# Optimization experiments

Measured on AMD Instinct MI355X. Metric: run time of the kernel, lower is better.

Reference implementation:

```python
import jax, jax.numpy as jnp
import numpy as np

N = 50000      # nodes
E = 800000     # edges
IN = 128       # in_channels
C = 32         # hidden_channels per head
H = 8          # heads
NC = 2         # num_classes
EPS = 1e-5     # batchnorm eps
SLOPE = 0.2    # leaky relu negative slope


def setup_inputs() -> dict:
    key = jax.random.key(0)
    ks = jax.random.split(key, 16)
    d = {}
    d["x"] = jax.random.normal(ks[0], (N, IN), dtype=jnp.float32)
    d["edge_index"] = jax.random.randint(ks[1], (2, E), 0, N, dtype=jnp.int64)
    # layer 0: IN -> H*C (concat)
    s0 = 1.0 / np.sqrt(IN)
    d["Wl0"] = jax.random.normal(ks[2], (IN, H * C), dtype=jnp.float32) * s0
    d["Wr0"] = jax.random.normal(ks[3], (IN, H * C), dtype=jnp.float32) * s0
    d["att0"] = jax.random.normal(ks[4], (H, C), dtype=jnp.float32) * (1.0 / np.sqrt(C))
    d["b0"] = jnp.zeros((H * C,), dtype=jnp.float32)
    d["g0"] = jnp.ones((H * C,), dtype=jnp.float32)
    d["be0"] = jnp.zeros((H * C,), dtype=jnp.float32)
    d["m0"] = jax.random.normal(ks[5], (H * C,), dtype=jnp.float32) * 0.1
    d["v0"] = jax.random.uniform(ks[6], (H * C,), dtype=jnp.float32, minval=0.5, maxval=1.5)
    # layer 1: H*C -> C (mean over heads, concat=False)
    s1 = 1.0 / np.sqrt(H * C)
    d["Wl1"] = jax.random.normal(ks[7], (H * C, H * C), dtype=jnp.float32) * s1
    d["Wr1"] = jax.random.normal(ks[8], (H * C, H * C), dtype=jnp.float32) * s1
    d["att1"] = jax.random.normal(ks[9], (H, C), dtype=jnp.float32) * (1.0 / np.sqrt(C))
    d["b1"] = jnp.zeros((C,), dtype=jnp.float32)
    d["g1"] = jnp.ones((C,), dtype=jnp.float32)
    d["be1"] = jnp.zeros((C,), dtype=jnp.float32)
    d["m1"] = jax.random.normal(ks[10], (C,), dtype=jnp.float32) * 0.1
    d["v1"] = jax.random.uniform(ks[11], (C,), dtype=jnp.float32, minval=0.5, maxval=1.5)
    # classifier C -> NC
    d["Wc"] = jax.random.normal(ks[12], (C, NC), dtype=jnp.float32) * (1.0 / np.sqrt(C))
    d["bc"] = jnp.zeros((NC,), dtype=jnp.float32)
    return d


def _gatv2_layer(x, src, dst, Wl, Wr, att, b, concat, num_nodes):
    # GATv2Conv (PyG semantics): x_l = source proj, x_r = target proj,
    # e_ij = att . LeakyReLU(x_l[j] + x_r[i]); softmax over incoming edges of i;
    # out_i = sum_j alpha_ij * x_l[j]. Self-loops are added (PyG default).
    nH, nC = att.shape
    xl = (x @ Wl).reshape(num_nodes, nH, nC)
    xr = (x @ Wr).reshape(num_nodes, nH, nC)
    e = xl[src] + xr[dst]                              # [E', H, C]
    e = jnp.where(e > 0, e, SLOPE * e)
    logits = jnp.einsum('ehc,hc->eh', e, att)          # [E', H]
    m = jax.ops.segment_max(logits, dst, num_segments=num_nodes)   # [N, H]
    ex = jnp.exp(logits - m[dst])
    denom = jax.ops.segment_sum(ex, dst, num_segments=num_nodes)   # [N, H]
    alpha = ex / denom[dst]                            # [E', H]
    msg = alpha[:, :, None] * xl[src]                  # [E', H, C]
    out = jax.ops.segment_sum(msg, dst, num_segments=num_nodes)    # [N, H, C]
    if concat:
        return out.reshape(num_nodes, nH * nC) + b
    return out.mean(axis=1) + b


def _bn(x, g, be, m, v):
    return (x - m) * jax.lax.rsqrt(v + EPS) * g + be


def reference(x, edge_index, Wl0, Wr0, att0, b0, g0, be0, m0, v0,
              Wl1, Wr1, att1, b1, g1, be1, m1, v1, Wc, bc):
    num_nodes = x.shape[0]
    loop = jnp.arange(num_nodes, dtype=edge_index.dtype)
    src = jnp.concatenate([edge_index[0], loop])
    dst = jnp.concatenate([edge_index[1], loop])
    h = _gatv2_layer(x, src, dst, Wl0, Wr0, att0, b0, True, num_nodes)
    h = _bn(h, g0, be0, m0, v0)
    h = jax.nn.elu(h)   # eval mode: dropout is identity
    h = _gatv2_layer(h, src, dst, Wl1, Wr1, att1, b1, False, num_nodes)
    h = _bn(h, g1, be1, m1, v1)
    return h @ Wc + bc
```

## Files before the change

kernel.cpp:

```cpp
#include <hip/hip_runtime.h>
#include <math.h>

#define N_NODES 50000
#define M_PAD   50048
#define E_EDGES 800000
#define IN_CH   128
#define C_CH    32
#define H_HEADS 8
#define HC      256
#define BN_EPS  1e-5f
#define SLOPE   0.2f

#define SCAN_CHUNK 512
#define SCAN_B     ((N_NODES + SCAN_CHUNK - 1) / SCAN_CHUNK)

typedef _Float16 f16x8 __attribute__((ext_vector_type(8)));
typedef _Float16 f16x4 __attribute__((ext_vector_type(4)));
typedef _Float16 f16x2 __attribute__((ext_vector_type(2)));
typedef float    f32x4 __attribute__((ext_vector_type(4)));


__global__ void k_init_deg(int* deg, int n) {
    int i = blockIdx.x * blockDim.x + threadIdx.x;
    if (i < n) deg[i] = 1;
}

__global__ void k_hist(const int* __restrict__ dst, int* deg, int e) {
    int i = blockIdx.x * blockDim.x + threadIdx.x;
    if (i < e) atomicAdd(&deg[dst[i]], 1);
}

__global__ __launch_bounds__(256) void k_scan_local(
        const int* __restrict__ deg, int* __restrict__ row_ptr,
        int* __restrict__ partials, int n) {
    __shared__ int sm[256];
    int t = threadIdx.x;
    int base = blockIdx.x * SCAN_CHUNK;
    int i0 = base + 2 * t, i1 = i0 + 1;
    int a = (i0 < n) ? deg[i0] : 0;
    int b = (i1 < n) ? deg[i1] : 0;
    int s = a + b;
    sm[t] = s;
    __syncthreads();
    #pragma unroll
    for (int off = 1; off < 256; off <<= 1) {
        int u = (t >= off) ? sm[t - off] : 0;
        __syncthreads();
        sm[t] += u;
        __syncthreads();
    }
    int excl = sm[t] - s;
    if (i0 < n) row_ptr[i0] = excl;
    if (i1 < n) row_ptr[i1] = excl + a;
    if (t == 255) partials[blockIdx.x] = sm[255];
}

__global__ __launch_bounds__(128) void k_scan_part(
        int* __restrict__ partials, int* __restrict__ row_ptr_n) {
    __shared__ int sm[128];
    int t = threadIdx.x;
    int v = (t < SCAN_B) ? partials[t] : 0;
    sm[t] = v;
    __syncthreads();
    #pragma unroll
    for (int off = 1; off < 128; off <<= 1) {
        int u = (t >= off) ? sm[t - off] : 0;
        __syncthreads();
        sm[t] += u;
        __syncthreads();
    }
    if (t < SCAN_B) partials[t] = sm[t] - v;
    if (t == 127) *row_ptr_n = sm[127];
}

__global__ void k_scan_add(int* __restrict__ row_ptr, int* __restrict__ cursor,
                           const int* __restrict__ partials, int n) {
    int i = blockIdx.x * blockDim.x + threadIdx.x;
    if (i < n) {
        int v = row_ptr[i] + partials[i / SCAN_CHUNK];
        row_ptr[i] = v;
        cursor[i] = v;
    }
}

__global__ void k_fill(const int* __restrict__ src, const int* __restrict__ dst,
                       int* cursor, int* csr_src, int e, int n) {
    int i = blockIdx.x * blockDim.x + threadIdx.x;
    if (i < e) {
        int d = dst[i];
        int p = atomicAdd(&cursor[d], 1);
        csr_src[p] = src[i];
    } else if (i < e + n) {
        int v = i - e;
        int p = atomicAdd(&cursor[v], 1);
        csr_src[p] = v;
    }
}


__global__ void k_split_x(const float* __restrict__ x, _Float16* __restrict__ xf) {
    int t = blockIdx.x * blockDim.x + threadIdx.x;
    if (t >= M_PAD * (IN_CH / 4)) return;
    int row = t / (IN_CH / 4);
    float4 v = {0.f, 0.f, 0.f, 0.f};
    if (row < N_NODES) v = ((const float4*)x)[t];
    f16x4 h = { (_Float16)v.x, (_Float16)v.y, (_Float16)v.z, (_Float16)v.w };
    ((f16x4*)xf)[t] = h;
}

__global__ void k_split_w(const float* __restrict__ W,
                          _Float16* __restrict__ wh, _Float16* __restrict__ wl,
                          int K, int N) {
    int t = blockIdx.x * blockDim.x + threadIdx.x;
    if (t >= K * N) return;
    int n = t / K, k = t - n * K;
    float v = W[(size_t)k * N + n];
    _Float16 h = (_Float16)v;
    wh[t] = h;
    wl[t] = (_Float16)(v - (float)h);
}


#define BK  32
#define LDA 40

__global__ __launch_bounds__(256) void k_gemm_mfma(
        const _Float16* __restrict__ A,
        const _Float16* __restrict__ W0h, const _Float16* __restrict__ W0l,
        const _Float16* __restrict__ W1h, const _Float16* __restrict__ W1l,
        _Float16* __restrict__ C0, _Float16* __restrict__ C1, int K) {
    const _Float16* Wh = blockIdx.z ? W1h : W0h;
    const _Float16* Wl = blockIdx.z ? W1l : W0l;
    _Float16* C = blockIdx.z ? C1 : C0;
    __shared__ _Float16 As[128 * LDA];
    __shared__ _Float16 Bh[128 * LDA], Bl[128 * LDA];
    int t = threadIdx.x;
    int lane = t & 63, wv = t >> 6;
    int quad = lane >> 4, r16 = lane & 15;
    size_t mBase = (size_t)blockIdx.x * 128;
    size_t nBase = (size_t)blockIdx.y * 128;
    int sr = t >> 2;
    int sc = (t & 3) * 8;
    f32x4 acc[2][8] = {};
    for (int k0 = 0; k0 < K; k0 += BK) {
        const _Float16* gA  = A + (mBase + sr) * K + k0 + sc;
        const _Float16* gBh = Wh + (nBase + sr) * K + k0 + sc;
        const _Float16* gBl = Wl + (nBase + sr) * K + k0 + sc;
        *(f16x8*)&As[sr * LDA + sc]        = *(const f16x8*)gA;
        *(f16x8*)&As[(sr + 64) * LDA + sc] = *(const f16x8*)(gA + (size_t)64 * K);
        *(f16x8*)&Bh[sr * LDA + sc]        = *(const f16x8*)gBh;
        *(f16x8*)&Bh[(sr + 64) * LDA + sc] = *(const f16x8*)(gBh + (size_t)64 * K);
        *(f16x8*)&Bl[sr * LDA + sc]        = *(const f16x8*)gBl;
        *(f16x8*)&Bl[(sr + 64) * LDA + sc] = *(const f16x8*)(gBl + (size_t)64 * K);
        __syncthreads();
        f16x8 av[2];
        #pragma unroll
        for (int mi = 0; mi < 2; ++mi) {
            int m = wv * 32 + mi * 16 + r16;
            av[mi] = *(f16x8*)&As[m * LDA + quad * 8];
        }
        #pragma unroll
        for (int ni = 0; ni < 8; ++ni) {
            int n = ni * 16 + r16;
            f16x8 bhv = *(f16x8*)&Bh[n * LDA + quad * 8];
            f16x8 blv = *(f16x8*)&Bl[n * LDA + quad * 8];
            #pragma unroll
            for (int mi = 0; mi < 2; ++mi) {
                acc[mi][ni] = __builtin_amdgcn_mfma_f32_16x16x32_f16(av[mi], bhv, acc[mi][ni], 0, 0, 0);
                acc[mi][ni] = __builtin_amdgcn_mfma_f32_16x16x32_f16(av[mi], blv, acc[mi][ni], 0, 0, 0);
            }
        }
        __syncthreads();
    }
    #pragma unroll
    for (int mi = 0; mi < 2; ++mi)
        #pragma unroll
        for (int r = 0; r < 4; ++r) {
            size_t row = mBase + wv * 32 + mi * 16 + quad * 4 + r;
            _Float16* cp = C + row * 256 + nBase + r16;
            #pragma unroll
            for (int ni = 0; ni < 8; ++ni)
                cp[ni * 16] = (_Float16)acc[mi][ni][r];
        }
}


__device__ __forceinline__ float edge_w16(f16x4 h, f16x4 xr, f16x4 att) {
    f16x4 e = h + xr;
    f16x4 es = e * (_Float16)SLOPE;
    f16x4 l = __builtin_elementwise_max(e, es);
#if __has_builtin(__builtin_amdgcn_fdot2)
    f16x2 l01 = __builtin_shufflevector(l, l, 0, 1);
    f16x2 l23 = __builtin_shufflevector(l, l, 2, 3);
    f16x2 a01 = __builtin_shufflevector(att, att, 0, 1);
    f16x2 a23 = __builtin_shufflevector(att, att, 2, 3);
    float p = __builtin_amdgcn_fdot2(l01, a01, 0.f, false);
    p = __builtin_amdgcn_fdot2(l23, a23, p, false);
#else
    float p = (float)l[0] * (float)att[0];
    p = fmaf((float)l[1], (float)att[1], p);
    p = fmaf((float)l[2], (float)att[2], p);
    p = fmaf((float)l[3], (float)att[3], p);
#endif
    p += __shfl_xor(p, 1);
    p += __shfl_xor(p, 2);
    p += __shfl_xor(p, 4);
    return __expf(p);
}

__device__ __forceinline__ float4 edge_accum(
        const f16x4* __restrict__ xl4, f16x4 xr_h, f16x4 att_h,
        const int* __restrict__ csr_src, int beg, int end, int lane) {
    const f16x4* xlp = xl4 + lane;
    float4 acc = {0.f, 0.f, 0.f, 0.f};
    float S = 0.f;
    int j = beg;
    for (; j + 4 <= end; j += 4) {
        int s0 = csr_src[j];
        int s1 = csr_src[j + 1];
        int s2 = csr_src[j + 2];
        int s3 = csr_src[j + 3];
        f16x4 h0 = xlp[(size_t)s0 * 64];
        f16x4 h1 = xlp[(size_t)s1 * 64];
        f16x4 h2 = xlp[(size_t)s2 * 64];
        f16x4 h3 = xlp[(size_t)s3 * 64];
        float w0 = edge_w16(h0, xr_h, att_h);
        float w1 = edge_w16(h1, xr_h, att_h);
        float w2 = edge_w16(h2, xr_h, att_h);
        float w3 = edge_w16(h3, xr_h, att_h);
        S += (w0 + w1) + (w2 + w3);
        acc.x = fmaf((float)h0[0], w0, acc.x); acc.y = fmaf((float)h0[1], w0, acc.y);
        acc.z = fmaf((float)h0[2], w0, acc.z); acc.w = fmaf((float)h0[3], w0, acc.w);
        acc.x = fmaf((float)h1[0], w1, acc.x); acc.y = fmaf((float)h1[1], w1, acc.y);
        acc.z = fmaf((float)h1[2], w1, acc.z); acc.w = fmaf((float)h1[3], w1, acc.w);
        acc.x = fmaf((float)h2[0], w2, acc.x); acc.y = fmaf((float)h2[1], w2, acc.y);
        acc.z = fmaf((float)h2[2], w2, acc.z); acc.w = fmaf((float)h2[3], w2, acc.w);
        acc.x = fmaf((float)h3[0], w3, acc.x); acc.y = fmaf((float)h3[1], w3, acc.y);
        acc.z = fmaf((float)h3[2], w3, acc.z); acc.w = fmaf((float)h3[3], w3, acc.w);
    }
    for (; j < end; ++j) {
        int s = csr_src[j];
        f16x4 hv = xlp[(size_t)s * 64];
        float w = edge_w16(hv, xr_h, att_h);
        S += w;
        acc.x = fmaf((float)hv[0], w, acc.x); acc.y = fmaf((float)hv[1], w, acc.y);
        acc.z = fmaf((float)hv[2], w, acc.z); acc.w = fmaf((float)hv[3], w, acc.w);
    }
    float inv = 1.f / S;
    acc.x *= inv; acc.y *= inv; acc.z *= inv; acc.w *= inv;
    return acc;
}

__device__ __forceinline__ f16x4 cvt_h4(float4 v) {
    f16x4 r = { (_Float16)v.x, (_Float16)v.y, (_Float16)v.z, (_Float16)v.w };
    return r;
}

__global__ __launch_bounds__(256) void k_edge0(
        const _Float16* __restrict__ xl, const _Float16* __restrict__ xr,
        const float* __restrict__ att,
        const int* __restrict__ row_ptr, const int* __restrict__ csr_src,
        const float* __restrict__ b0, const float* __restrict__ g0,
        const float* __restrict__ be0, const float* __restrict__ m0,
        const float* __restrict__ v0,
        _Float16* __restrict__ h0) {
    int lane = threadIdx.x & 63;
    int i = blockIdx.x * 4 + (threadIdx.x >> 6);
    const f16x4* xl4 = (const f16x4*)xl;
    f16x4 xr_h = ((const f16x4*)xr)[(size_t)i * 64 + lane];
    f16x4 att_h = cvt_h4(((const float4*)att)[lane]);
    int beg = row_ptr[i], end = row_ptr[i + 1];
    float4 r = edge_accum(xl4, xr_h, att_h, csr_src, beg, end, lane);
    float4 bb = ((const float4*)b0)[lane];
    float4 gg = ((const float4*)g0)[lane];
    float4 ee = ((const float4*)be0)[lane];
    float4 mm = ((const float4*)m0)[lane];
    float4 vv = ((const float4*)v0)[lane];
    float4 o;
    o.x = (r.x + bb.x - mm.x) * rsqrtf(vv.x + BN_EPS) * gg.x + ee.x;
    o.y = (r.y + bb.y - mm.y) * rsqrtf(vv.y + BN_EPS) * gg.y + ee.y;
    o.z = (r.z + bb.z - mm.z) * rsqrtf(vv.z + BN_EPS) * gg.z + ee.z;
    o.w = (r.w + bb.w - mm.w) * rsqrtf(vv.w + BN_EPS) * gg.w + ee.w;
    o.x = o.x > 0.f ? o.x : expm1f(o.x);
    o.y = o.y > 0.f ? o.y : expm1f(o.y);
    o.z = o.z > 0.f ? o.z : expm1f(o.z);
    o.w = o.w > 0.f ? o.w : expm1f(o.w);
    f16x4 hh = { (_Float16)o.x, (_Float16)o.y, (_Float16)o.z, (_Float16)o.w };
    ((f16x4*)h0)[(size_t)i * 64 + lane] = hh;
}

__global__ __launch_bounds__(256) void k_edge1(
        const _Float16* __restrict__ xl, const _Float16* __restrict__ xr,
        const float* __restrict__ att,
        const int* __restrict__ row_ptr, const int* __restrict__ csr_src,
        const float* __restrict__ b1, const float* __restrict__ g1,
        const float* __restrict__ be1, const float* __restrict__ m1,
        const float* __restrict__ v1,
        const float* __restrict__ Wc, const float* __restrict__ bc,
        float* __restrict__ out) {
    int lane = threadIdx.x & 63;
    int q = lane & 7;
    int i = blockIdx.x * 4 + (threadIdx.x >> 6);
    const f16x4* xl4 = (const f16x4*)xl;
    f16x4 xr_h = ((const f16x4*)xr)[(size_t)i * 64 + lane];
    f16x4 att_h = cvt_h4(((const float4*)att)[lane]);
    int beg = row_ptr[i], end = row_ptr[i + 1];
    float4 r = edge_accum(xl4, xr_h, att_h, csr_src, beg, end, lane);
    #pragma unroll
    for (int mask = 8; mask <= 32; mask <<= 1) {
        r.x += __shfl_xor(r.x, mask);
        r.y += __shfl_xor(r.y, mask);
        r.z += __shfl_xor(r.z, mask);
        r.w += __shfl_xor(r.w, mask);
    }
    float4 bb = ((const float4*)b1)[q];
    float4 gg = ((const float4*)g1)[q];
    float4 ee = ((const float4*)be1)[q];
    float4 mm = ((const float4*)m1)[q];
    float4 vv = ((const float4*)v1)[q];
    r.x = (r.x * 0.125f + bb.x - mm.x) * rsqrtf(vv.x + BN_EPS) * gg.x + ee.x;
    r.y = (r.y * 0.125f + bb.y - mm.y) * rsqrtf(vv.y + BN_EPS) * gg.y + ee.y;
    r.z = (r.z * 0.125f + bb.z - mm.z) * rsqrtf(vv.z + BN_EPS) * gg.z + ee.z;
    r.w = (r.w * 0.125f + bb.w - mm.w) * rsqrtf(vv.w + BN_EPS) * gg.w + ee.w;
    float4 wc0 = ((const float4*)Wc)[q * 2];
    float4 wc1 = ((const float4*)Wc)[q * 2 + 1];
    float o0 = r.x * wc0.x + r.y * wc0.z + r.z * wc1.x + r.w * wc1.z;
    float o1 = r.x * wc0.y + r.y * wc0.w + r.z * wc1.y + r.w * wc1.w;
    #pragma unroll
    for (int mask = 1; mask <= 4; mask <<= 1) {
        o0 += __shfl_xor(o0, mask);
        o1 += __shfl_xor(o1, mask);
    }
    if (lane == 0) {
        float2 ov = {o0 + bc[0], o1 + bc[1]};
        *(float2*)(out + (size_t)i * 2) = ov;
    }
}


extern "C" void kernel_launch(void* const* d_in, const int* in_sizes, int n_in,
                              void* d_out, int out_size, void* d_ws, size_t ws_size,
                              hipStream_t stream) {
    const float* x    = (const float*)d_in[0];
    const int*   ei   = (const int*)d_in[1];
    const float* Wl0  = (const float*)d_in[2];
    const float* Wr0  = (const float*)d_in[3];
    const float* att0 = (const float*)d_in[4];
    const float* b0   = (const float*)d_in[5];
    const float* g0   = (const float*)d_in[6];
    const float* be0  = (const float*)d_in[7];
    const float* m0   = (const float*)d_in[8];
    const float* v0   = (const float*)d_in[9];
    const float* Wl1  = (const float*)d_in[10];
    const float* Wr1  = (const float*)d_in[11];
    const float* att1 = (const float*)d_in[12];
    const float* b1   = (const float*)d_in[13];
    const float* g1   = (const float*)d_in[14];
    const float* be1  = (const float*)d_in[15];
    const float* m1   = (const float*)d_in[16];
    const float* v1   = (const float*)d_in[17];
    const float* Wc   = (const float*)d_in[18];
    const float* bc   = (const float*)d_in[19];
    float* out = (float*)d_out;

    const int N = N_NODES, E = E_EDGES;
    const int* srcp = ei;
    const int* dstp = ei + E;

    char* p = (char*)d_ws;
    _Float16* xlf = (_Float16*)p; p += (size_t)M_PAD * HC * 2;
    _Float16* xrf = (_Float16*)p; p += (size_t)M_PAD * HC * 2;
    char* shared0 = p; p += (size_t)M_PAD * HC * 2;
    _Float16* h0 = (_Float16*)shared0;
    _Float16* xf = (_Float16*)shared0;
    _Float16* W0lh = (_Float16*)p; p += (size_t)HC * IN_CH * 2;
    _Float16* W0ll = (_Float16*)p; p += (size_t)HC * IN_CH * 2;
    _Float16* W0rh = (_Float16*)p; p += (size_t)HC * IN_CH * 2;
    _Float16* W0rl = (_Float16*)p; p += (size_t)HC * IN_CH * 2;
    _Float16* W1lh = (_Float16*)p; p += (size_t)HC * HC * 2;
    _Float16* W1ll = (_Float16*)p; p += (size_t)HC * HC * 2;
    _Float16* W1rh = (_Float16*)p; p += (size_t)HC * HC * 2;
    _Float16* W1rl = (_Float16*)p; p += (size_t)HC * HC * 2;
    int* deg      = (int*)p;
    int* row_ptr  = deg + N;
    int* cursor   = row_ptr + (N + 1);
    int* partials = cursor + N;
    int* csr_src  = partials + ((SCAN_B + 3) & ~3);

    k_init_deg<<<(N + 255) / 256, 256, 0, stream>>>(deg, N);
    k_hist<<<(E + 255) / 256, 256, 0, stream>>>(dstp, deg, E);
    k_scan_local<<<SCAN_B, 256, 0, stream>>>(deg, row_ptr, partials, N);
    k_scan_part<<<1, 128, 0, stream>>>(partials, row_ptr + N);
    k_scan_add<<<(N + 255) / 256, 256, 0, stream>>>(row_ptr, cursor, partials, N);
    k_fill<<<(E + N + 255) / 256, 256, 0, stream>>>(srcp, dstp, cursor, csr_src, E, N);

    k_split_x<<<(M_PAD * (IN_CH / 4) + 255) / 256, 256, 0, stream>>>(x, xf);
    k_split_w<<<(IN_CH * HC + 255) / 256, 256, 0, stream>>>(Wl0, W0lh, W0ll, IN_CH, HC);
    k_split_w<<<(IN_CH * HC + 255) / 256, 256, 0, stream>>>(Wr0, W0rh, W0rl, IN_CH, HC);
    k_split_w<<<(HC * HC + 255) / 256, 256, 0, stream>>>(Wl1, W1lh, W1ll, HC, HC);
    k_split_w<<<(HC * HC + 255) / 256, 256, 0, stream>>>(Wr1, W1rh, W1rl, HC, HC);

    dim3 ggrid(M_PAD / 128, 2, 2);
    k_gemm_mfma<<<ggrid, 256, 0, stream>>>(xf, W0lh, W0ll, W0rh, W0rl,
                                           xlf, xrf, IN_CH);
    k_edge0<<<N / 4, 256, 0, stream>>>(xlf, xrf, att0, row_ptr, csr_src,
                                       b0, g0, be0, m0, v0, h0);
    k_gemm_mfma<<<ggrid, 256, 0, stream>>>(h0, W1lh, W1ll, W1rh, W1rl,
                                           xlf, xrf, HC);
    k_edge1<<<N / 4, 256, 0, stream>>>(xlf, xrf, att1, row_ptr, csr_src,
                                       b1, g1, be1, m1, v1, Wc, bc, out);
}
```

Before: 426.4 us.

## Drop fp16 weight residual split and fuse x conversion into GEMM loads

Removes the hi/lo fp16 split of the weights, so each GEMM issues half as many MFMAs and stages one B tile instead of two. The layer-0 GEMM now reads fp32 x directly and converts it to fp16 while loading into shared memory, which removes the separate conversion kernel and its extra pass over memory. The four weight-transpose launches are merged into one kernel. In exchange, the weights lose the low-order correction and are rounded to fp16, which lowers GEMM accuracy.

```diff
diff --git a/kernel.cpp b/kernel.cpp
--- a/kernel.cpp
+++ b/kernel.cpp
@@ -98,42 +98,39 @@
 }
 
 
-__global__ void k_split_x(const float* __restrict__ x, _Float16* __restrict__ xf) {
+__global__ void k_split_w4(const float* __restrict__ Wl0, const float* __restrict__ Wr0,
+                           const float* __restrict__ Wl1, const float* __restrict__ Wr1,
+                           _Float16* __restrict__ W0lt, _Float16* __restrict__ W0rt,
+                           _Float16* __restrict__ W1lt, _Float16* __restrict__ W1rt) {
     int t = blockIdx.x * blockDim.x + threadIdx.x;
-    if (t >= M_PAD * (IN_CH / 4)) return;
-    int row = t / (IN_CH / 4);
-    float4 v = {0.f, 0.f, 0.f, 0.f};
-    if (row < N_NODES) v = ((const float4*)x)[t];
-    f16x4 h = { (_Float16)v.x, (_Float16)v.y, (_Float16)v.z, (_Float16)v.w };
-    ((f16x4*)xf)[t] = h;
-}
-
-__global__ void k_split_w(const float* __restrict__ W,
-                          _Float16* __restrict__ wh, _Float16* __restrict__ wl,
-                          int K, int N) {
-    int t = blockIdx.x * blockDim.x + threadIdx.x;
-    if (t >= K * N) return;
-    int n = t / K, k = t - n * K;
-    float v = W[(size_t)k * N + n];
-    _Float16 h = (_Float16)v;
-    wh[t] = h;
-    wl[t] = (_Float16)(v - (float)h);
+    const float* W; _Float16* O; int K, rel;
+    if (t < 32768)       { W = Wl0; O = W0lt; K = 128; rel = t; }
+    else if (t < 65536)  { W = Wr0; O = W0rt; K = 128; rel = t - 32768; }
+    else if (t < 131072) { W = Wl1; O = W1lt; K = 256; rel = t - 65536; }
+    else if (t < 196608) { W = Wr1; O = W1rt; K = 256; rel = t - 131072; }
+    else return;
+    int n = rel / K, k = rel - n * K;
+    O[rel] = (_Float16)W[(size_t)k * 256 + n];
 }
 
 
 #define BK  32
 #define LDA 40
 
+__device__ __forceinline__ f16x8 cvt_h8(float4 a, float4 b) {
+    f16x8 v = { (_Float16)a.x, (_Float16)a.y, (_Float16)a.z, (_Float16)a.w,
+                (_Float16)b.x, (_Float16)b.y, (_Float16)b.z, (_Float16)b.w };
+    return v;
+}
+
 __global__ __launch_bounds__(256) void k_gemm_mfma(
-        const _Float16* __restrict__ A,
-        const _Float16* __restrict__ W0h, const _Float16* __restrict__ W0l,
-        const _Float16* __restrict__ W1h, const _Float16* __restrict__ W1l,
+        const _Float16* __restrict__ A16, const float* __restrict__ A32,
+        const _Float16* __restrict__ W0t, const _Float16* __restrict__ W1t,
         _Float16* __restrict__ C0, _Float16* __restrict__ C1, int K) {
-    const _Float16* Wh = blockIdx.z ? W1h : W0h;
-    const _Float16* Wl = blockIdx.z ? W1l : W0l;
+    const _Float16* Wt = blockIdx.z ? W1t : W0t;
     _Float16* C = blockIdx.z ? C1 : C0;
     __shared__ _Float16 As[128 * LDA];
-    __shared__ _Float16 Bh[128 * LDA], Bl[128 * LDA];
+    __shared__ _Float16 Bs[128 * LDA];
     int t = threadIdx.x;
     int lane = t & 63, wv = t >> 6;
     int quad = lane >> 4, r16 = lane & 15;
@@ -143,15 +140,29 @@
     int sc = (t & 3) * 8;
     f32x4 acc[2][8] = {};
     for (int k0 = 0; k0 < K; k0 += BK) {
-        const _Float16* gA  = A + (mBase + sr) * K + k0 + sc;
-        const _Float16* gBh = Wh + (nBase + sr) * K + k0 + sc;
-        const _Float16* gBl = Wl + (nBase + sr) * K + k0 + sc;
-        *(f16x8*)&As[sr * LDA + sc]        = *(const f16x8*)gA;
-        *(f16x8*)&As[(sr + 64) * LDA + sc] = *(const f16x8*)(gA + (size_t)64 * K);
-        *(f16x8*)&Bh[sr * LDA + sc]        = *(const f16x8*)gBh;
-        *(f16x8*)&Bh[(sr + 64) * LDA + sc] = *(const f16x8*)(gBh + (size_t)64 * K);
-        *(f16x8*)&Bl[sr * LDA + sc]        = *(const f16x8*)gBl;
-        *(f16x8*)&Bl[(sr + 64) * LDA + sc] = *(const f16x8*)(gBl + (size_t)64 * K);
+        if (A32) {
+            size_t r0 = mBase + sr, r1 = r0 + 64;
+            float4 a0 = {0.f,0.f,0.f,0.f}, a1 = a0, b0 = a0, b1 = a0;
+            if (r0 < N_NODES) {
+                const float* g = A32 + r0 * K + k0 + sc;
+                a0 = ((const float4*)g)[0];
+                a1 = ((const float4*)g)[1];
+            }
+            if (r1 < N_NODES) {
+                const float* g = A32 + r1 * K + k0 + sc;
+                b0 = ((const float4*)g)[0];
+                b1 = ((const float4*)g)[1];
+            }
+            *(f16x8*)&As[sr * LDA + sc]        = cvt_h8(a0, a1);
+            *(f16x8*)&As[(sr + 64) * LDA + sc] = cvt_h8(b0, b1);
+        } else {
+            const _Float16* gA = A16 + (mBase + sr) * K + k0 + sc;
+            *(f16x8*)&As[sr * LDA + sc]        = *(const f16x8*)gA;
+            *(f16x8*)&As[(sr + 64) * LDA + sc] = *(const f16x8*)(gA + (size_t)64 * K);
+        }
+        const _Float16* gB = Wt + (nBase + sr) * K + k0 + sc;
+        *(f16x8*)&Bs[sr * LDA + sc]        = *(const f16x8*)gB;
+        *(f16x8*)&Bs[(sr + 64) * LDA + sc] = *(const f16x8*)(gB + (size_t)64 * K);
         __syncthreads();
         f16x8 av[2];
         #pragma unroll
@@ -162,13 +173,10 @@
         #pragma unroll
         for (int ni = 0; ni < 8; ++ni) {
             int n = ni * 16 + r16;
-            f16x8 bhv = *(f16x8*)&Bh[n * LDA + quad * 8];
-            f16x8 blv = *(f16x8*)&Bl[n * LDA + quad * 8];
+            f16x8 bv = *(f16x8*)&Bs[n * LDA + quad * 8];
             #pragma unroll
-            for (int mi = 0; mi < 2; ++mi) {
-                acc[mi][ni] = __builtin_amdgcn_mfma_f32_16x16x32_f16(av[mi], bhv, acc[mi][ni], 0, 0, 0);
-                acc[mi][ni] = __builtin_amdgcn_mfma_f32_16x16x32_f16(av[mi], blv, acc[mi][ni], 0, 0, 0);
-            }
+            for (int mi = 0; mi < 2; ++mi)
+                acc[mi][ni] = __builtin_amdgcn_mfma_f32_16x16x32_f16(av[mi], bv, acc[mi][ni], 0, 0, 0);
         }
         __syncthreads();
     }
@@ -370,17 +378,11 @@
     char* p = (char*)d_ws;
     _Float16* xlf = (_Float16*)p; p += (size_t)M_PAD * HC * 2;
     _Float16* xrf = (_Float16*)p; p += (size_t)M_PAD * HC * 2;
-    char* shared0 = p; p += (size_t)M_PAD * HC * 2;
-    _Float16* h0 = (_Float16*)shared0;
-    _Float16* xf = (_Float16*)shared0;
-    _Float16* W0lh = (_Float16*)p; p += (size_t)HC * IN_CH * 2;
-    _Float16* W0ll = (_Float16*)p; p += (size_t)HC * IN_CH * 2;
-    _Float16* W0rh = (_Float16*)p; p += (size_t)HC * IN_CH * 2;
-    _Float16* W0rl = (_Float16*)p; p += (size_t)HC * IN_CH * 2;
-    _Float16* W1lh = (_Float16*)p; p += (size_t)HC * HC * 2;
-    _Float16* W1ll = (_Float16*)p; p += (size_t)HC * HC * 2;
-    _Float16* W1rh = (_Float16*)p; p += (size_t)HC * HC * 2;
-    _Float16* W1rl = (_Float16*)p; p += (size_t)HC * HC * 2;
+    _Float16* h0  = (_Float16*)p; p += (size_t)M_PAD * HC * 2;
+    _Float16* W0lt = (_Float16*)p; p += (size_t)HC * IN_CH * 2;
+    _Float16* W0rt = (_Float16*)p; p += (size_t)HC * IN_CH * 2;
+    _Float16* W1lt = (_Float16*)p; p += (size_t)HC * HC * 2;
+    _Float16* W1rt = (_Float16*)p; p += (size_t)HC * HC * 2;
     int* deg      = (int*)p;
     int* row_ptr  = deg + N;
     int* cursor   = row_ptr + (N + 1);
@@ -394,19 +396,13 @@
     k_scan_add<<<(N + 255) / 256, 256, 0, stream>>>(row_ptr, cursor, partials, N);
     k_fill<<<(E + N + 255) / 256, 256, 0, stream>>>(srcp, dstp, cursor, csr_src, E, N);
 
-    k_split_x<<<(M_PAD * (IN_CH / 4) + 255) / 256, 256, 0, stream>>>(x, xf);
-    k_split_w<<<(IN_CH * HC + 255) / 256, 256, 0, stream>>>(Wl0, W0lh, W0ll, IN_CH, HC);
-    k_split_w<<<(IN_CH * HC + 255) / 256, 256, 0, stream>>>(Wr0, W0rh, W0rl, IN_CH, HC);
-    k_split_w<<<(HC * HC + 255) / 256, 256, 0, stream>>>(Wl1, W1lh, W1ll, HC, HC);
-    k_split_w<<<(HC * HC + 255) / 256, 256, 0, stream>>>(Wr1, W1rh, W1rl, HC, HC);
+    k_split_w4<<<768, 256, 0, stream>>>(Wl0, Wr0, Wl1, Wr1, W0lt, W0rt, W1lt, W1rt);
 
     dim3 ggrid(M_PAD / 128, 2, 2);
-    k_gemm_mfma<<<ggrid, 256, 0, stream>>>(xf, W0lh, W0ll, W0rh, W0rl,
-                                           xlf, xrf, IN_CH);
+    k_gemm_mfma<<<ggrid, 256, 0, stream>>>(nullptr, x, W0lt, W0rt, xlf, xrf, IN_CH);
     k_edge0<<<N / 4, 256, 0, stream>>>(xlf, xrf, att0, row_ptr, csr_src,
                                        b0, g0, be0, m0, v0, h0);
-    k_gemm_mfma<<<ggrid, 256, 0, stream>>>(h0, W1lh, W1ll, W1rh, W1rl,
-                                           xlf, xrf, HC);
+    k_gemm_mfma<<<ggrid, 256, 0, stream>>>(h0, nullptr, W1lt, W1rt, xlf, xrf, HC);
     k_edge1<<<N / 4, 256, 0, stream>>>(xlf, xrf, att1, row_ptr, csr_src,
                                        b1, g1, be1, m1, v1, Wc, bc, out);
 }
```

After: 408.4 us, median of 2. 1.04x faster.
